# Kernel optimization log

Hardware: AMD Instinct MI355X
Metric: run time of the kernel (lower is better)

Reference implementation:

```python
import jax, jax.numpy as jnp
import numpy as np

FEAT = 512
ACT_NUMS = (8, 6, 4)            # actions per categorical type
SUM_ACT = sum(ACT_NUMS)          # 18
STARTS = np.cumsum([0] + list(ACT_NUMS[:-1]))  # [0, 8, 14]
FC_HIDDEN, FC_OUT = 140, 256


def setup_inputs() -> dict:
    key = jax.random.key(0)
    ks = jax.random.split(key, 10)
    F, A = 2048, 32
    s = 0.02
    return {
        "current_feature": jax.random.normal(ks[0], (F, A, FEAT), jnp.float32),
        "next_feature": jax.random.normal(ks[1], (F, A, FEAT), jnp.float32),
        "actions": jax.random.randint(ks[2], (F, 3, A), 0, 4),
        "W1": jax.random.normal(ks[3], (FEAT + SUM_ACT, FC_HIDDEN), jnp.float32) * s,
        "b1": jnp.zeros((FC_HIDDEN,), jnp.float32),
        "W2": jax.random.normal(ks[4], (FC_HIDDEN, FC_OUT), jnp.float32) * s,
        "b2": jnp.zeros((FC_OUT,), jnp.float32),
        "Wi0": jax.random.normal(ks[5], (2 * FEAT, ACT_NUMS[0]), jnp.float32) * s,
        "bi0": jnp.zeros((ACT_NUMS[0],), jnp.float32),
        "Wi1": jax.random.normal(ks[6], (2 * FEAT, ACT_NUMS[1]), jnp.float32) * s,
        "bi1": jnp.zeros((ACT_NUMS[1],), jnp.float32),
        "Wi2": jax.random.normal(ks[7], (2 * FEAT, ACT_NUMS[2]), jnp.float32) * s,
        "bi2": jnp.zeros((ACT_NUMS[2],), jnp.float32),
    }


def reference(current_feature, next_feature, actions,
              W1, b1, W2, b2, Wi0, bi0, Wi1, bi1, Wi2, bi2):
    dt = current_feature.dtype
    starts = jnp.asarray(STARTS, dtype=actions.dtype)  # [3]
    # Vectorized replacement of the triple nested scatter loop:
    # global index per (frame, type, agent), one-hot over SUM_ACT, summed over types
    # (per-type index ranges are disjoint, so sum == set).
    idx = actions + starts[None, :, None]                       # [F, T, A]
    action_one_hot = jax.nn.one_hot(idx, SUM_ACT, dtype=dt).sum(axis=1)  # [F, A, S]

    # Forward dynamics: fwd_net = Linear -> Linear (no nonlinearity, per source)
    fwd_in = jnp.concatenate([current_feature, action_one_hot], axis=2)  # [F, A, FEAT+S]
    next_feature_pred = (fwd_in @ W1 + b1) @ W2 + b2                     # [F, A, 256]

    # Inverse dynamics: per-action-type Linear + Softmax(dim=1)
    # (nn.Softmax(dim=1) on a 3D tensor normalizes over the agent axis -- kept faithful)
    inv_in = jnp.concatenate([current_feature, next_feature], axis=2)    # [F, A, 2*FEAT]
    a0 = jax.nn.softmax(inv_in @ Wi0 + bi0, axis=1)
    a1 = jax.nn.softmax(inv_in @ Wi1 + bi1, axis=1)
    a2 = jax.nn.softmax(inv_in @ Wi2 + bi2, axis=1)
    return (next_feature_pred, a0, a1, a2)
```

## Files before the change

kernel.cpp:

```cpp
#include <hip/hip_runtime.h>


using bf16x8  = __attribute__((ext_vector_type(8))) __bf16;
using floatx4 = __attribute__((ext_vector_type(4))) float;

__device__ __forceinline__ unsigned short f2bf(float f) {
    unsigned int u = __float_as_uint(f);
    unsigned int r = (u + 0x7fffu + ((u >> 16) & 1u)) >> 16;
    return (unsigned short)r;
}
__device__ __forceinline__ ushort4 cvt4(const float* __restrict__ p) {
    float4 v = *(const float4*)p;
    ushort4 o;
    o.x = f2bf(v.x); o.y = f2bf(v.y); o.z = f2bf(v.z); o.w = f2bf(v.w);
    return o;
}

#define M_ROWS 65536
#define HP 160

#define OFF_W1T 0
#define OFF_W2T (OFF_W1T + 144*512)
#define OFF_WCT (OFF_W2T + 256*160)
#define OFF_H   (OFF_WCT + 32*1024)

#define OFF_A0 ((size_t)16777216)
#define OFF_A1 ((size_t)17301504)
#define OFF_A2 ((size_t)17694720)

__global__ __launch_bounds__(256) void prep_kernel(
    const float* __restrict__ W1,
    const float* __restrict__ W2,
    const float* __restrict__ Wi0,
    const float* __restrict__ Wi1,
    const float* __restrict__ Wi2,
    unsigned short* __restrict__ ws)
{
    unsigned short* W1T = ws + OFF_W1T;
    unsigned short* W2T = ws + OFF_W2T;
    unsigned short* WcT = ws + OFF_WCT;
    const int total = 144*512 + 256*160 + 32*1024;
    for (int idx = blockIdx.x * 256 + threadIdx.x; idx < total; idx += gridDim.x * 256) {
        if (idx < 144*512) {
            int j = idx >> 9, k = idx & 511;
            W1T[idx] = (j < 140) ? f2bf(W1[k*140 + j]) : (unsigned short)0;
        } else if (idx < 144*512 + 256*160) {
            int i2 = idx - 144*512;
            int n = i2 / 160, k = i2 - n*160;
            W2T[i2] = (k < 140) ? f2bf(W2[k*256 + n]) : (unsigned short)0;
        } else {
            int i3 = idx - (144*512 + 256*160);
            int j = i3 >> 10, k = i3 & 1023;
            unsigned short v = 0;
            if (j < 8)       v = f2bf(Wi0[k*8 + j]);
            else if (j < 14) v = f2bf(Wi1[k*6 + (j - 8)]);
            else if (j < 18) v = f2bf(Wi2[k*4 + (j - 14)]);
            WcT[i3] = v;
        }
    }
}

__global__ __launch_bounds__(256) void gemm1_kernel(
    const float* __restrict__ cf,
    const int* __restrict__ actions,
    const float* __restrict__ W1,
    const float* __restrict__ b1,
    const unsigned short* __restrict__ W1T,
    unsigned short* __restrict__ hbuf)
{
    __shared__ alignas(16) __bf16 As[64 * 72];
    __shared__ alignas(16) __bf16 Bs[144 * 72];
    __shared__ float Us[18 * 144];
    __shared__ float b1s[144];
    __shared__ int   sidx[64 * 3];

    const int t = threadIdx.x;
    const int w = t >> 6, l = t & 63;
    const int m0 = blockIdx.x * 64;

    for (int i = t; i < 18 * 144; i += 256) {
        int s = i / 144, j = i - s * 144;
        Us[i] = (j < 140) ? W1[(512 + s) * 140 + j] : 0.f;
    }
    if (t < 144) b1s[t] = (t < 140) ? b1[t] : 0.f;
    if (t < 192) {
        int r = t / 3, tt = t - r * 3;
        int m = m0 + r, f = m >> 5, a = m & 31;
        int start = (tt == 0) ? 0 : (tt == 1 ? 8 : 14);
        sidx[t] = actions[f * 96 + tt * 32 + a] + start;
    }

    floatx4 acc[9];
#pragma unroll
    for (int n = 0; n < 9; ++n) { acc[n][0]=0.f; acc[n][1]=0.f; acc[n][2]=0.f; acc[n][3]=0.f; }

    for (int kc = 0; kc < 8; ++kc) {
#pragma unroll
        for (int it = 0; it < 4; ++it) {
            int idx = t + it * 256;
            int r = idx >> 4, c4 = idx & 15;
            *(ushort4*)(&As[r * 72 + c4 * 4]) =
                cvt4(cf + (size_t)(m0 + r) * 512 + kc * 64 + c4 * 4);
        }
#pragma unroll
        for (int it = 0; it < 5; ++it) {
            int idx = t + it * 256;
            if (idx < 1152) {
                int j = idx >> 3, c8 = idx & 7;
                *(uint4*)(&Bs[j * 72 + c8 * 8]) =
                    *(const uint4*)(W1T + (size_t)j * 512 + kc * 64 + c8 * 8);
            }
        }
        __syncthreads();
        const int ao = (w * 16 + (l & 15)) * 72 + ((l >> 4) << 3);
#pragma unroll
        for (int ks = 0; ks < 2; ++ks) {
            bf16x8 a = *(const bf16x8*)&As[ao + ks * 32];
#pragma unroll
            for (int n = 0; n < 9; ++n) {
                bf16x8 b = *(const bf16x8*)&Bs[(n * 16 + (l & 15)) * 72 + ks * 32 + ((l >> 4) << 3)];
                acc[n] = __builtin_amdgcn_mfma_f32_16x16x32_bf16(a, b, acc[n], 0, 0, 0);
            }
        }
        __syncthreads();
    }

    const int col = l & 15;
    const int r0 = w * 16 + ((l >> 4) << 2);
#pragma unroll
    for (int i = 0; i < 4; ++i) {
        int r = r0 + i;
        int s0 = sidx[r * 3 + 0], s1 = sidx[r * 3 + 1], s2 = sidx[r * 3 + 2];
        size_t rowbase = (size_t)(m0 + r) * HP;
#pragma unroll
        for (int n = 0; n < 9; ++n) {
            int j = n * 16 + col;
            float v = acc[n][i] + b1s[j]
                    + Us[s0 * 144 + j] + Us[s1 * 144 + j] + Us[s2 * 144 + j];
            hbuf[rowbase + j] = f2bf(v);
        }
    }
    {
        int r = t >> 2, g = t & 3;
        ushort4 z; z.x = z.y = z.z = z.w = 0;
        *(ushort4*)(hbuf + (size_t)(m0 + r) * HP + 144 + g * 4) = z;
    }
}

__global__ __launch_bounds__(256) void gemm2_kernel(
    const unsigned short* __restrict__ hbuf,
    const float* __restrict__ b2,
    const unsigned short* __restrict__ W2T,
    float* __restrict__ outp)
{
    __shared__ alignas(16) __bf16 hs[64 * 56];
    __shared__ alignas(16) __bf16 Ws[256 * 56];
    __shared__ float b2s[256];

    const int t = threadIdx.x;
    const int w = t >> 6, l = t & 63;
    const int m0 = blockIdx.x * 64;

    b2s[t] = b2[t];

    floatx4 acc[16];
#pragma unroll
    for (int n = 0; n < 16; ++n) { acc[n][0]=0.f; acc[n][1]=0.f; acc[n][2]=0.f; acc[n][3]=0.f; }

    for (int kc = 0; kc < 5; ++kc) {
        {
            int r = t >> 2, c8 = t & 3;
            *(uint4*)(&hs[r * 56 + c8 * 8]) =
                *(const uint4*)(hbuf + (size_t)(m0 + r) * HP + kc * 32 + c8 * 8);
        }
#pragma unroll
        for (int it = 0; it < 4; ++it) {
            int idx = t + it * 256;
            int n = idx >> 2, c8 = idx & 3;
            *(uint4*)(&Ws[n * 56 + c8 * 8]) =
                *(const uint4*)(W2T + (size_t)n * 160 + kc * 32 + c8 * 8);
        }
        __syncthreads();
        bf16x8 a = *(const bf16x8*)&hs[(w * 16 + (l & 15)) * 56 + ((l >> 4) << 3)];
#pragma unroll
        for (int n = 0; n < 16; ++n) {
            bf16x8 b = *(const bf16x8*)&Ws[(n * 16 + (l & 15)) * 56 + ((l >> 4) << 3)];
            acc[n] = __builtin_amdgcn_mfma_f32_16x16x32_bf16(a, b, acc[n], 0, 0, 0);
        }
        __syncthreads();
    }

    const int col = l & 15;
    const int r0 = w * 16 + ((l >> 4) << 2);
#pragma unroll
    for (int n = 0; n < 16; ++n) {
        int j = n * 16 + col;
        float bj = b2s[j];
#pragma unroll
        for (int i = 0; i < 4; ++i)
            outp[(size_t)(m0 + r0 + i) * 256 + j] = acc[n][i] + bj;
    }
}

__global__ __launch_bounds__(256) void inv_kernel(
    const float* __restrict__ cf,
    const float* __restrict__ nf,
    const unsigned short* __restrict__ WcT,
    float* __restrict__ out_base)
{
    __shared__ alignas(16) __bf16 As[64 * 72];
    __shared__ alignas(16) __bf16 Bs[32 * 72];
    __shared__ float Ls[64 * 20];
    __shared__ float rmx[36], rsc[36];

    const int t = threadIdx.x;
    const int w = t >> 6, l = t & 63;
    const int m0 = blockIdx.x * 64;

    floatx4 acc[2];
#pragma unroll
    for (int n = 0; n < 2; ++n) { acc[n][0]=0.f; acc[n][1]=0.f; acc[n][2]=0.f; acc[n][3]=0.f; }

    for (int kc = 0; kc < 16; ++kc) {
        const float* src = (kc < 8) ? cf : nf;
        const int ko = (kc & 7) * 64;
#pragma unroll
        for (int it = 0; it < 4; ++it) {
            int idx = t + it * 256;
            int r = idx >> 4, c4 = idx & 15;
            *(ushort4*)(&As[r * 72 + c4 * 4]) =
                cvt4(src + (size_t)(m0 + r) * 512 + ko + c4 * 4);
        }
        {
            int j = t >> 3, c8 = t & 7;
            *(uint4*)(&Bs[j * 72 + c8 * 8]) =
                *(const uint4*)(WcT + (size_t)j * 1024 + kc * 64 + c8 * 8);
        }
        __syncthreads();
#pragma unroll
        for (int ks = 0; ks < 2; ++ks) {
            bf16x8 a = *(const bf16x8*)&As[(w * 16 + (l & 15)) * 72 + ks * 32 + ((l >> 4) << 3)];
#pragma unroll
            for (int n = 0; n < 2; ++n) {
                bf16x8 b = *(const bf16x8*)&Bs[(n * 16 + (l & 15)) * 72 + ks * 32 + ((l >> 4) << 3)];
                acc[n] = __builtin_amdgcn_mfma_f32_16x16x32_bf16(a, b, acc[n], 0, 0, 0);
            }
        }
        __syncthreads();
    }

    const int col = l & 15;
    const int r0 = w * 16 + ((l >> 4) << 2);
#pragma unroll
    for (int n = 0; n < 2; ++n) {
        int j = n * 16 + col;
        if (j < 18) {
#pragma unroll
            for (int i = 0; i < 4; ++i) Ls[(r0 + i) * 20 + j] = acc[n][i];
        }
    }
    __syncthreads();

    if (t < 36) {
        int fr = t / 18, j = t - fr * 18;
        float mx = -1e30f;
        for (int a = 0; a < 32; ++a) mx = fmaxf(mx, Ls[(fr * 32 + a) * 20 + j]);
        float s = 0.f;
        for (int a = 0; a < 32; ++a) s += expf(Ls[(fr * 32 + a) * 20 + j] - mx);
        rmx[t] = mx; rsc[t] = 1.f / s;
    }
    __syncthreads();

#pragma unroll
    for (int it = 0; it < 5; ++it) {
        int idx = t + it * 256;
        if (idx < 1152) {
            int r = idx / 18, j = idx - r * 18;
            int fr = r >> 5;
            float v = expf(Ls[r * 20 + j] - rmx[fr * 18 + j]) * rsc[fr * 18 + j];
            int m = m0 + r;
            size_t o;
            if (j < 8)       o = OFF_A0 + (size_t)m * 8 + j;
            else if (j < 14) o = OFF_A1 + (size_t)m * 6 + (j - 8);
            else             o = OFF_A2 + (size_t)m * 4 + (j - 14);
            out_base[o] = v;
        }
    }
}

extern "C" void kernel_launch(void* const* d_in, const int* in_sizes, int n_in,
                              void* d_out, int out_size, void* d_ws, size_t ws_size,
                              hipStream_t stream)
{
    const float* cf  = (const float*)d_in[0];
    const float* nf  = (const float*)d_in[1];
    const int*   act = (const int*)d_in[2];
    const float* W1  = (const float*)d_in[3];
    const float* b1  = (const float*)d_in[4];
    const float* W2  = (const float*)d_in[5];
    const float* b2  = (const float*)d_in[6];
    const float* Wi0 = (const float*)d_in[7];
    const float* Wi1 = (const float*)d_in[9];
    const float* Wi2 = (const float*)d_in[11];

    unsigned short* ws   = (unsigned short*)d_ws;
    unsigned short* W1T  = ws + OFF_W1T;
    unsigned short* W2T  = ws + OFF_W2T;
    unsigned short* WcT  = ws + OFF_WCT;
    unsigned short* hbuf = ws + OFF_H;
    float* outp = (float*)d_out;

    hipLaunchKernelGGL(prep_kernel, dim3(256), dim3(256), 0, stream,
                       W1, W2, Wi0, Wi1, Wi2, ws);
    hipLaunchKernelGGL(gemm1_kernel, dim3(M_ROWS / 64), dim3(256), 0, stream,
                       cf, act, W1, b1, W1T, hbuf);
    hipLaunchKernelGGL(gemm2_kernel, dim3(M_ROWS / 64), dim3(256), 0, stream,
                       hbuf, b2, W2T, outp);
    hipLaunchKernelGGL(inv_kernel, dim3(M_ROWS / 64), dim3(256), 0, stream,
                       cf, nf, WcT, outp);
}
```

Baseline: 387.4 us.

## Fuse forward and inverse GEMMs into one kernel with fragment-packed weights

Merges the three kernels (hidden GEMM, output GEMM, inverse-dynamics GEMM plus softmax) into one fused kernel. The hidden activations now stay in shared memory instead of going through a global buffer, and current_feature is read once for both the forward and inverse paths. The prep kernel lays weights out in MFMA fragment order, so each lane loads its B operand straight from global/L2 and the per-step shared-memory staging and barriers go away. The cost is more accumulator registers per thread, which may lower occupancy, and the A operand is loaded per lane as strided 32-byte reads with no staging.

Result: no change. 389.2 us (+0.4%).

```diff
diff --git a/kernel.cpp b/kernel.cpp
--- a/kernel.cpp
+++ b/kernel.cpp
@@ -6,23 +6,20 @@
 
 __device__ __forceinline__ unsigned short f2bf(float f) {
     unsigned int u = __float_as_uint(f);
-    unsigned int r = (u + 0x7fffu + ((u >> 16) & 1u)) >> 16;
-    return (unsigned short)r;
-}
-__device__ __forceinline__ ushort4 cvt4(const float* __restrict__ p) {
-    float4 v = *(const float4*)p;
-    ushort4 o;
-    o.x = f2bf(v.x); o.y = f2bf(v.y); o.z = f2bf(v.z); o.w = f2bf(v.w);
-    return o;
-}
-
-#define M_ROWS 65536
-#define HP 160
-
-#define OFF_W1T 0
-#define OFF_W2T (OFF_W1T + 144*512)
-#define OFF_WCT (OFF_W2T + 256*160)
-#define OFF_H   (OFF_WCT + 32*1024)
+    return (unsigned short)((u + 0x7fffu + ((u >> 16) & 1u)) >> 16);
+}
+__device__ __forceinline__ bf16x8 cvt8(const float* __restrict__ p) {
+    float4 x = *(const float4*)p;
+    float4 y = *(const float4*)(p + 4);
+    union { bf16x8 v; unsigned short s[8]; } u;
+    u.s[0] = f2bf(x.x); u.s[1] = f2bf(x.y); u.s[2] = f2bf(x.z); u.s[3] = f2bf(x.w);
+    u.s[4] = f2bf(y.x); u.s[5] = f2bf(y.y); u.s[6] = f2bf(y.z); u.s[7] = f2bf(y.w);
+    return u.v;
+}
+
+#define OFF_W1P 0
+#define OFF_W2P (OFF_W1P + 16*9*512)
+#define OFF_WCP (OFF_W2P + 5*16*512)
 
 #define OFF_A0 ((size_t)16777216)
 #define OFF_A1 ((size_t)17301504)
@@ -36,227 +33,155 @@
     const float* __restrict__ Wi2,
     unsigned short* __restrict__ ws)
 {
-    unsigned short* W1T = ws + OFF_W1T;
-    unsigned short* W2T = ws + OFF_W2T;
-    unsigned short* WcT = ws + OFF_WCT;
-    const int total = 144*512 + 256*160 + 32*1024;
+    const int T1 = 16*9*512;
+    const int T2 = T1 + 5*16*512;
+    const int total = T2 + 32*2*512;
     for (int idx = blockIdx.x * 256 + threadIdx.x; idx < total; idx += gridDim.x * 256) {
-        if (idx < 144*512) {
-            int j = idx >> 9, k = idx & 511;
-            W1T[idx] = (j < 140) ? f2bf(W1[k*140 + j]) : (unsigned short)0;
-        } else if (idx < 144*512 + 256*160) {
-            int i2 = idx - 144*512;
-            int n = i2 / 160, k = i2 - n*160;
-            W2T[i2] = (k < 140) ? f2bf(W2[k*256 + n]) : (unsigned short)0;
+        unsigned short v = 0;
+        if (idx < T1) {
+            int e = idx & 7, l = (idx >> 3) & 63;
+            int n = (idx >> 9) % 9, kc = idx / (9*512);
+            int k = kc*32 + ((l >> 4) << 3) + e, j = n*16 + (l & 15);
+            if (j < 140) v = f2bf(W1[k*140 + j]);
+            ws[OFF_W1P + idx] = v;
+        } else if (idx < T2) {
+            int i2 = idx - T1;
+            int e = i2 & 7, l = (i2 >> 3) & 63;
+            int n = (i2 >> 9) & 15, kc = i2 >> 13;
+            int k = kc*32 + ((l >> 4) << 3) + e, j = n*16 + (l & 15);
+            if (k < 140) v = f2bf(W2[k*256 + j]);
+            ws[OFF_W2P + i2] = v;
         } else {
-            int i3 = idx - (144*512 + 256*160);
-            int j = i3 >> 10, k = i3 & 1023;
-            unsigned short v = 0;
+            int i3 = idx - T2;
+            int e = i3 & 7, l = (i3 >> 3) & 63;
+            int n = (i3 >> 9) & 1, kc = i3 >> 10;
+            int k = kc*32 + ((l >> 4) << 3) + e, j = n*16 + (l & 15);
             if (j < 8)       v = f2bf(Wi0[k*8 + j]);
             else if (j < 14) v = f2bf(Wi1[k*6 + (j - 8)]);
             else if (j < 18) v = f2bf(Wi2[k*4 + (j - 14)]);
-            WcT[i3] = v;
-        }
-    }
-}
-
-__global__ __launch_bounds__(256) void gemm1_kernel(
+            ws[OFF_WCP + i3] = v;
+        }
+    }
+}
+
+__global__ __launch_bounds__(256) void fused_kernel(
     const float* __restrict__ cf,
+    const float* __restrict__ nf,
     const int* __restrict__ actions,
     const float* __restrict__ W1,
     const float* __restrict__ b1,
-    const unsigned short* __restrict__ W1T,
-    unsigned short* __restrict__ hbuf)
+    const float* __restrict__ b2,
+    const unsigned short* __restrict__ ws,
+    float* __restrict__ outp)
 {
-    __shared__ alignas(16) __bf16 As[64 * 72];
-    __shared__ alignas(16) __bf16 Bs[144 * 72];
+    __shared__ alignas(16) __bf16 hs[64 * 168];
     __shared__ float Us[18 * 144];
     __shared__ float b1s[144];
-    __shared__ int   sidx[64 * 3];
-
-    const int t = threadIdx.x;
-    const int w = t >> 6, l = t & 63;
+    __shared__ float b2s[256];
+    __shared__ float Ls[64 * 20];
+    __shared__ float rmx[36], rsc[36];
+    __shared__ int   sidx[192];
+
+    const int t = threadIdx.x, w = t >> 6, l = t & 63;
     const int m0 = blockIdx.x * 64;
+    const int q = l >> 4, col = l & 15;
+    const unsigned short* W1P = ws + OFF_W1P;
+    const unsigned short* W2P = ws + OFF_W2P;
+    const unsigned short* WCP = ws + OFF_WCP;
 
     for (int i = t; i < 18 * 144; i += 256) {
         int s = i / 144, j = i - s * 144;
         Us[i] = (j < 140) ? W1[(512 + s) * 140 + j] : 0.f;
     }
     if (t < 144) b1s[t] = (t < 140) ? b1[t] : 0.f;
+    b2s[t] = b2[t];
     if (t < 192) {
         int r = t / 3, tt = t - r * 3;
-        int m = m0 + r, f = m >> 5, a = m & 31;
+        int m = m0 + r;
         int start = (tt == 0) ? 0 : (tt == 1 ? 8 : 14);
-        sidx[t] = actions[f * 96 + tt * 32 + a] + start;
-    }
-
-    floatx4 acc[9];
-#pragma unroll
-    for (int n = 0; n < 9; ++n) { acc[n][0]=0.f; acc[n][1]=0.f; acc[n][2]=0.f; acc[n][3]=0.f; }
-
-    for (int kc = 0; kc < 8; ++kc) {
-#pragma unroll
-        for (int it = 0; it < 4; ++it) {
-            int idx = t + it * 256;
-            int r = idx >> 4, c4 = idx & 15;
-            *(ushort4*)(&As[r * 72 + c4 * 4]) =
-                cvt4(cf + (size_t)(m0 + r) * 512 + kc * 64 + c4 * 4);
-        }
-#pragma unroll
-        for (int it = 0; it < 5; ++it) {
-            int idx = t + it * 256;
-            if (idx < 1152) {
-                int j = idx >> 3, c8 = idx & 7;
-                *(uint4*)(&Bs[j * 72 + c8 * 8]) =
-                    *(const uint4*)(W1T + (size_t)j * 512 + kc * 64 + c8 * 8);
-            }
-        }
-        __syncthreads();
-        const int ao = (w * 16 + (l & 15)) * 72 + ((l >> 4) << 3);
-#pragma unroll
-        for (int ks = 0; ks < 2; ++ks) {
-            bf16x8 a = *(const bf16x8*)&As[ao + ks * 32];
-#pragma unroll
-            for (int n = 0; n < 9; ++n) {
-                bf16x8 b = *(const bf16x8*)&Bs[(n * 16 + (l & 15)) * 72 + ks * 32 + ((l >> 4) << 3)];
-                acc[n] = __builtin_amdgcn_mfma_f32_16x16x32_bf16(a, b, acc[n], 0, 0, 0);
-            }
-        }
-        __syncthreads();
-    }
-
-    const int col = l & 15;
-    const int r0 = w * 16 + ((l >> 4) << 2);
+        sidx[t] = actions[(m >> 5) * 96 + tt * 32 + (m & 31)] + start;
+    }
+
+    const float* cfr = cf + (size_t)(m0 + w * 16 + col) * 512 + q * 8;
+    const float* nfr = nf + (size_t)(m0 + w * 16 + col) * 512 + q * 8;
+
+    floatx4 acc1[9], acc3[2];
+#pragma unroll
+    for (int n = 0; n < 9; ++n) { acc1[n][0]=0.f; acc1[n][1]=0.f; acc1[n][2]=0.f; acc1[n][3]=0.f; }
+#pragma unroll
+    for (int n = 0; n < 2; ++n) { acc3[n][0]=0.f; acc3[n][1]=0.f; acc3[n][2]=0.f; acc3[n][3]=0.f; }
+
+    for (int kc = 0; kc < 16; ++kc) {
+        bf16x8 av = cvt8(cfr + kc * 32);
+        const unsigned short* bp = W1P + (size_t)(kc * 9) * 512 + l * 8;
+#pragma unroll
+        for (int n = 0; n < 9; ++n)
+            acc1[n] = __builtin_amdgcn_mfma_f32_16x16x32_bf16(
+                av, *(const bf16x8*)(bp + n * 512), acc1[n], 0, 0, 0);
+        const unsigned short* cp = WCP + (size_t)(kc * 2) * 512 + l * 8;
+        acc3[0] = __builtin_amdgcn_mfma_f32_16x16x32_bf16(
+            av, *(const bf16x8*)(cp), acc3[0], 0, 0, 0);
+        acc3[1] = __builtin_amdgcn_mfma_f32_16x16x32_bf16(
+            av, *(const bf16x8*)(cp + 512), acc3[1], 0, 0, 0);
+    }
+
+    for (int kc = 0; kc < 16; ++kc) {
+        bf16x8 av = cvt8(nfr + kc * 32);
+        const unsigned short* cp = WCP + (size_t)((16 + kc) * 2) * 512 + l * 8;
+        acc3[0] = __builtin_amdgcn_mfma_f32_16x16x32_bf16(
+            av, *(const bf16x8*)(cp), acc3[0], 0, 0, 0);
+        acc3[1] = __builtin_amdgcn_mfma_f32_16x16x32_bf16(
+            av, *(const bf16x8*)(cp + 512), acc3[1], 0, 0, 0);
+    }
+
+    __syncthreads();
+
+    const int r0 = w * 16 + (q << 2);
 #pragma unroll
     for (int i = 0; i < 4; ++i) {
-        int r = r0 + i;
-        int s0 = sidx[r * 3 + 0], s1 = sidx[r * 3 + 1], s2 = sidx[r * 3 + 2];
-        size_t rowbase = (size_t)(m0 + r) * HP;
+        int rr = r0 + i;
+        int s0 = sidx[rr * 3], s1 = sidx[rr * 3 + 1], s2 = sidx[rr * 3 + 2];
 #pragma unroll
         for (int n = 0; n < 9; ++n) {
             int j = n * 16 + col;
-            float v = acc[n][i] + b1s[j]
-                    + Us[s0 * 144 + j] + Us[s1 * 144 + j] + Us[s2 * 144 + j];
-            hbuf[rowbase + j] = f2bf(v);
+            float v = acc1[n][i] + b1s[j] + Us[s0 * 144 + j] + Us[s1 * 144 + j] + Us[s2 * 144 + j];
+            ((unsigned short*)hs)[rr * 168 + j] = f2bf(v);
         }
     }
     {
-        int r = t >> 2, g = t & 3;
+        int rr = t >> 2, g = t & 3;
         ushort4 z; z.x = z.y = z.z = z.w = 0;
-        *(ushort4*)(hbuf + (size_t)(m0 + r) * HP + 144 + g * 4) = z;
-    }
-}
-
-__global__ __launch_bounds__(256) void gemm2_kernel(
-    const unsigned short* __restrict__ hbuf,
-    const float* __restrict__ b2,
-    const unsigned short* __restrict__ W2T,
-    float* __restrict__ outp)
-{
-    __shared__ alignas(16) __bf16 hs[64 * 56];
-    __shared__ alignas(16) __bf16 Ws[256 * 56];
-    __shared__ float b2s[256];
-
-    const int t = threadIdx.x;
-    const int w = t >> 6, l = t & 63;
-    const int m0 = blockIdx.x * 64;
-
-    b2s[t] = b2[t];
-
-    floatx4 acc[16];
-#pragma unroll
-    for (int n = 0; n < 16; ++n) { acc[n][0]=0.f; acc[n][1]=0.f; acc[n][2]=0.f; acc[n][3]=0.f; }
+        *(ushort4*)((unsigned short*)hs + rr * 168 + 144 + g * 4) = z;
+    }
+    __syncthreads();
+
+    floatx4 acc2[16];
+#pragma unroll
+    for (int n = 0; n < 16; ++n) { acc2[n][0]=0.f; acc2[n][1]=0.f; acc2[n][2]=0.f; acc2[n][3]=0.f; }
 
     for (int kc = 0; kc < 5; ++kc) {
-        {
-            int r = t >> 2, c8 = t & 3;
-            *(uint4*)(&hs[r * 56 + c8 * 8]) =
-                *(const uint4*)(hbuf + (size_t)(m0 + r) * HP + kc * 32 + c8 * 8);
-        }
-#pragma unroll
-        for (int it = 0; it < 4; ++it) {
-            int idx = t + it * 256;
-            int n = idx >> 2, c8 = idx & 3;
-            *(uint4*)(&Ws[n * 56 + c8 * 8]) =
-                *(const uint4*)(W2T + (size_t)n * 160 + kc * 32 + c8 * 8);
-        }
-        __syncthreads();
-        bf16x8 a = *(const bf16x8*)&hs[(w * 16 + (l & 15)) * 56 + ((l >> 4) << 3)];
-#pragma unroll
-        for (int n = 0; n < 16; ++n) {
-            bf16x8 b = *(const bf16x8*)&Ws[(n * 16 + (l & 15)) * 56 + ((l >> 4) << 3)];
-            acc[n] = __builtin_amdgcn_mfma_f32_16x16x32_bf16(a, b, acc[n], 0, 0, 0);
-        }
-        __syncthreads();
-    }
-
-    const int col = l & 15;
-    const int r0 = w * 16 + ((l >> 4) << 2);
+        bf16x8 av = *(const bf16x8*)&hs[(w * 16 + col) * 168 + kc * 32 + q * 8];
+        const unsigned short* bp = W2P + (size_t)(kc * 16) * 512 + l * 8;
+#pragma unroll
+        for (int n = 0; n < 16; ++n)
+            acc2[n] = __builtin_amdgcn_mfma_f32_16x16x32_bf16(
+                av, *(const bf16x8*)(bp + n * 512), acc2[n], 0, 0, 0);
+    }
 #pragma unroll
     for (int n = 0; n < 16; ++n) {
         int j = n * 16 + col;
         float bj = b2s[j];
 #pragma unroll
         for (int i = 0; i < 4; ++i)
-            outp[(size_t)(m0 + r0 + i) * 256 + j] = acc[n][i] + bj;
-    }
-}
-
-__global__ __launch_bounds__(256) void inv_kernel(
-    const float* __restrict__ cf,
-    const float* __restrict__ nf,
-    const unsigned short* __restrict__ WcT,
-    float* __restrict__ out_base)
-{
-    __shared__ alignas(16) __bf16 As[64 * 72];
-    __shared__ alignas(16) __bf16 Bs[32 * 72];
-    __shared__ float Ls[64 * 20];
-    __shared__ float rmx[36], rsc[36];
-
-    const int t = threadIdx.x;
-    const int w = t >> 6, l = t & 63;
-    const int m0 = blockIdx.x * 64;
-
-    floatx4 acc[2];
-#pragma unroll
-    for (int n = 0; n < 2; ++n) { acc[n][0]=0.f; acc[n][1]=0.f; acc[n][2]=0.f; acc[n][3]=0.f; }
-
-    for (int kc = 0; kc < 16; ++kc) {
-        const float* src = (kc < 8) ? cf : nf;
-        const int ko = (kc & 7) * 64;
-#pragma unroll
-        for (int it = 0; it < 4; ++it) {
-            int idx = t + it * 256;
-            int r = idx >> 4, c4 = idx & 15;
-            *(ushort4*)(&As[r * 72 + c4 * 4]) =
-                cvt4(src + (size_t)(m0 + r) * 512 + ko + c4 * 4);
-        }
-        {
-            int j = t >> 3, c8 = t & 7;
-            *(uint4*)(&Bs[j * 72 + c8 * 8]) =
-                *(const uint4*)(WcT + (size_t)j * 1024 + kc * 64 + c8 * 8);
-        }
-        __syncthreads();
-#pragma unroll
-        for (int ks = 0; ks < 2; ++ks) {
-            bf16x8 a = *(const bf16x8*)&As[(w * 16 + (l & 15)) * 72 + ks * 32 + ((l >> 4) << 3)];
-#pragma unroll
-            for (int n = 0; n < 2; ++n) {
-                bf16x8 b = *(const bf16x8*)&Bs[(n * 16 + (l & 15)) * 72 + ks * 32 + ((l >> 4) << 3)];
-                acc[n] = __builtin_amdgcn_mfma_f32_16x16x32_bf16(a, b, acc[n], 0, 0, 0);
-            }
-        }
-        __syncthreads();
-    }
-
-    const int col = l & 15;
-    const int r0 = w * 16 + ((l >> 4) << 2);
+            outp[(size_t)(m0 + r0 + i) * 256 + j] = acc2[n][i] + bj;
+    }
+
 #pragma unroll
     for (int n = 0; n < 2; ++n) {
         int j = n * 16 + col;
         if (j < 18) {
 #pragma unroll
-            for (int i = 0; i < 4; ++i) Ls[(r0 + i) * 20 + j] = acc[n][i];
+            for (int i = 0; i < 4; ++i) Ls[(r0 + i) * 20 + j] = acc3[n][i];
         }
     }
     __syncthreads();
@@ -283,7 +208,7 @@
             if (j < 8)       o = OFF_A0 + (size_t)m * 8 + j;
             else if (j < 14) o = OFF_A1 + (size_t)m * 6 + (j - 8);
             else             o = OFF_A2 + (size_t)m * 4 + (j - 14);
-            out_base[o] = v;
+            outp[o] = v;
         }
     }
 }
@@ -303,19 +228,11 @@
     const float* Wi1 = (const float*)d_in[9];
     const float* Wi2 = (const float*)d_in[11];
 
-    unsigned short* ws   = (unsigned short*)d_ws;
-    unsigned short* W1T  = ws + OFF_W1T;
-    unsigned short* W2T  = ws + OFF_W2T;
-    unsigned short* WcT  = ws + OFF_WCT;
-    unsigned short* hbuf = ws + OFF_H;
+    unsigned short* ws = (unsigned short*)d_ws;
     float* outp = (float*)d_out;
 
-    hipLaunchKernelGGL(prep_kernel, dim3(256), dim3(256), 0, stream,
+    hipLaunchKernelGGL(prep_kernel, dim3(144), dim3(256), 0, stream,
                        W1, W2, Wi0, Wi1, Wi2, ws);
-    hipLaunchKernelGGL(gemm1_kernel, dim3(M_ROWS / 64), dim3(256), 0, stream,
-                       cf, act, W1, b1, W1T, hbuf);
-    hipLaunchKernelGGL(gemm2_kernel, dim3(M_ROWS / 64), dim3(256), 0, stream,
-                       hbuf, b2, W2T, outp);
-    hipLaunchKernelGGL(inv_kernel, dim3(M_ROWS / 64), dim3(256), 0, stream,
-                       cf, nf, WcT, outp);
-}
+    hipLaunchKernelGGL(fused_kernel, dim3(1024), dim3(256), 0, stream,
+                       cf, nf, act, W1, b1, b2, ws, outp);
+}
```
